# Kernel tuning notes

Measured on AMD Instinct MI355X. Metric: run time of the kernel, lower is better.

Reference implementation:

```python
import jax, jax.numpy as jnp
import numpy as np

IN_DIM = 256
OUT_DIM = 256
NUM_HEADS = 8
HEAD_DIM = OUT_DIM // NUM_HEADS
EPS = 1e-5


def setup_inputs() -> dict:
    key = jax.random.key(0)
    ks = jax.random.split(key, 12)
    B, N = 8, 1024
    s_in = 1.0 / np.sqrt(IN_DIM)
    s_out = 1.0 / np.sqrt(OUT_DIM)
    return {
        "node_features": jax.random.normal(ks[0], (B, N, IN_DIM), jnp.float32),
        "edge_weights": jax.random.uniform(ks[1], (B, N, N), jnp.float32),
        "Wq": jax.random.normal(ks[2], (IN_DIM, OUT_DIM), jnp.float32) * s_in,
        "bq": jnp.zeros((OUT_DIM,), jnp.float32),
        "Wk": jax.random.normal(ks[3], (IN_DIM, OUT_DIM), jnp.float32) * s_in,
        "bk": jnp.zeros((OUT_DIM,), jnp.float32),
        "Wv": jax.random.normal(ks[4], (IN_DIM, OUT_DIM), jnp.float32) * s_in,
        "bv": jnp.zeros((OUT_DIM,), jnp.float32),
        "We": jax.random.normal(ks[5], (NUM_HEADS,), jnp.float32),  # edge_proj: Linear(1, H)
        "be": jnp.zeros((NUM_HEADS,), jnp.float32),
        "Wo": jax.random.normal(ks[6], (OUT_DIM, OUT_DIM), jnp.float32) * s_out,
        "bo": jnp.zeros((OUT_DIM,), jnp.float32),
        "gamma": jnp.ones((OUT_DIM,), jnp.float32),
        "beta": jnp.zeros((OUT_DIM,), jnp.float32),
    }


def reference(node_features, edge_weights, Wq, bq, Wk, bk, Wv, bv, We, be, Wo, bo, gamma, beta):
    B, N, _ = node_features.shape
    H, D = NUM_HEADS, HEAD_DIM
    # QKV projections -> (B, N, H, D)
    Q = (node_features @ Wq + bq).reshape(B, N, H, D)
    K = (node_features @ Wk + bk).reshape(B, N, H, D)
    V = (node_features @ Wv + bv).reshape(B, N, H, D)
    # scores: (B, H, N, N)
    scores = jnp.einsum("bnhd,bmhd->bhnm", Q, K) / jnp.sqrt(jnp.float32(D))
    # edge bias: Linear(1->H) applied to distance matrix, permuted to (B,H,N,N)
    edge_bias = edge_weights[:, None, :, :] * We[None, :, None, None] + be[None, :, None, None]
    attn = jax.nn.softmax(scores + edge_bias, axis=-1)
    out = jnp.einsum("bhnm,bmhd->bnhd", attn, V).reshape(B, N, H * D)
    out = out @ Wo + bo
    # residual (in_dim == out_dim) + LayerNorm
    x = node_features + out
    mu = jnp.mean(x, axis=-1, keepdims=True)
    var = jnp.mean(jnp.square(x - mu), axis=-1, keepdims=True)
    return (x - mu) * jax.lax.rsqrt(var + EPS) * gamma + beta
```

## Files before the change

kernel.cpp:

```cpp
#include <hip/hip_runtime.h>

#define NB   8
#define NN   1024
#define DIN  256
#define DOUT 256
#define NH   8
#define DH   32
constexpr float LN_EPS   = 1e-5f;
constexpr float QK_SCALE = 0.17677669529663687f;

typedef __attribute__((ext_vector_type(8))) short s16x8;
typedef __attribute__((ext_vector_type(4))) float f32x4;

__device__ __forceinline__ unsigned short f2bf(float f) {
    unsigned int u = __float_as_uint(f);
    u += 0x7FFFu + ((u >> 16) & 1u);
    return (unsigned short)(u >> 16);
}
__device__ __forceinline__ float bf2f(unsigned short h) {
    return __uint_as_float(((unsigned int)h) << 16);
}
__device__ __forceinline__ unsigned int packbf(float a, float b) {
    return (unsigned int)f2bf(a) | ((unsigned int)f2bf(b) << 16);
}

__global__ __launch_bounds__(256) void qkv_kernel(
    const float* __restrict__ X,
    const float* __restrict__ Wq, const float* __restrict__ bq,
    const float* __restrict__ Wk, const float* __restrict__ bk,
    const float* __restrict__ Wv, const float* __restrict__ bv,
    unsigned short* __restrict__ Qhig, unsigned short* __restrict__ Qlog,
    unsigned short* __restrict__ Kbg,  float* __restrict__ Vf)
{
    const int m0 = blockIdx.x * 64;
    const int n0 = blockIdx.y * 64;
    const int t  = threadIdx.x;
    const int tc = t & 15, tr = t >> 4;

    __shared__ float Xs[32][68];
    __shared__ float Ws[3][32][68];

    float acc[3][4][4];
#pragma unroll
    for (int j = 0; j < 4; ++j) {
        float b0 = bq[n0 + tc*4 + j];
        float b1 = bk[n0 + tc*4 + j];
        float b2 = bv[n0 + tc*4 + j];
#pragma unroll
        for (int i = 0; i < 4; ++i) { acc[0][i][j] = b0; acc[1][i][j] = b1; acc[2][i][j] = b2; }
    }

    const int xrow = t >> 2, xseg = (t & 3) * 8;
    const int wrow = t >> 3, wseg = (t & 7) * 8;

    for (int k0 = 0; k0 < DIN; k0 += 32) {
        __syncthreads();
        {
            const float* src = X + (m0 + xrow) * DIN + k0 + xseg;
            float tmp[8];
            *(float4*)&tmp[0] = *(const float4*)(src);
            *(float4*)&tmp[4] = *(const float4*)(src + 4);
#pragma unroll
            for (int c = 0; c < 8; ++c) Xs[xseg + c][xrow] = tmp[c];
        }
#pragma unroll
        for (int w = 0; w < 3; ++w) {
            const float* Wp  = (w == 0) ? Wq : (w == 1) ? Wk : Wv;
            const float* src = Wp + (k0 + wrow) * DOUT + n0 + wseg;
            *(float4*)&Ws[w][wrow][wseg]     = *(const float4*)(src);
            *(float4*)&Ws[w][wrow][wseg + 4] = *(const float4*)(src + 4);
        }
        __syncthreads();
#pragma unroll
        for (int kk = 0; kk < 32; ++kk) {
            float4 x4 = *(const float4*)&Xs[kk][tr*4];
            float xr[4] = {x4.x, x4.y, x4.z, x4.w};
#pragma unroll
            for (int w = 0; w < 3; ++w) {
                float4 w4 = *(const float4*)&Ws[w][kk][tc*4];
                float wr[4] = {w4.x, w4.y, w4.z, w4.w};
#pragma unroll
                for (int i = 0; i < 4; ++i)
#pragma unroll
                    for (int j = 0; j < 4; ++j)
                        acc[w][i][j] = fmaf(xr[i], wr[j], acc[w][i][j]);
            }
        }
    }

    const int c0 = n0 + tc*4;
    const int h = c0 >> 5, d0 = c0 & 31;
#pragma unroll
    for (int i = 0; i < 4; ++i) {
        int row = m0 + tr*4 + i;
        int b = row >> 10, n = row & (NN - 1);
        size_t base = ((size_t)(b*NH + h)*NN + n)*DH + d0;
        ushort4 qh, ql, kb;
#pragma unroll
        for (int j = 0; j < 4; ++j) {
            float q = acc[0][i][j] * QK_SCALE;
            unsigned short hb = f2bf(q);
            float lo = q - bf2f(hb);
            ((unsigned short*)&qh)[j] = hb;
            ((unsigned short*)&ql)[j] = f2bf(lo);
            ((unsigned short*)&kb)[j] = f2bf(acc[1][i][j]);
        }
        *(ushort4*)&Qhig[base] = qh;
        *(ushort4*)&Qlog[base] = ql;
        *(ushort4*)&Kbg[base]  = kb;
        *(float4*)&Vf[base] = make_float4(acc[2][i][0], acc[2][i][1], acc[2][i][2], acc[2][i][3]);
    }
}

__global__ __launch_bounds__(256) void vtrans_kernel(
    const float* __restrict__ Vf, unsigned short* __restrict__ Vt)
{
    const int bid = blockIdx.x;
    const int c  = bid & 15;
    const int bh = bid >> 4;
    const int t  = threadIdx.x;
    __shared__ float T[64][33];
    {
        const int n = t >> 2, seg = (t & 3) * 8;
        const float* src = Vf + ((size_t)bh*NN + c*64 + n)*DH + seg;
        float4 a = *(const float4*)src;
        float4 b4 = *(const float4*)(src + 4);
        T[n][seg+0]=a.x;  T[n][seg+1]=a.y;  T[n][seg+2]=a.z;  T[n][seg+3]=a.w;
        T[n][seg+4]=b4.x; T[n][seg+5]=b4.y; T[n][seg+6]=b4.z; T[n][seg+7]=b4.w;
    }
    __syncthreads();
    {
        const int dh = t >> 3, nb = (t & 7) * 8;
        unsigned short o[8];
#pragma unroll
        for (int i = 0; i < 8; ++i) o[i] = f2bf(T[nb + i][dh]);
        *(s16x8*)&Vt[((size_t)bh*DH + dh)*NN + c*64 + nb] = *(const s16x8*)o;
    }
}

__global__ __launch_bounds__(256) void attn_kernel(
    const unsigned short* __restrict__ Qhi, const unsigned short* __restrict__ Qlo,
    const unsigned short* __restrict__ Kb,  const unsigned short* __restrict__ Vt,
    const float* __restrict__ Eg, const float* __restrict__ We,
    float* __restrict__ AO)
{
    const int bid = blockIdx.x;
    const int b  = bid & 7;
    const int h  = (bid >> 3) & 7;
    const int qt = bid >> 6;
    const int q0 = qt * 64;
    const int t    = threadIdx.x;
    const int lane = t & 63;
    const int wid  = t >> 6;
    const int l15  = lane & 15;
    const int hi   = lane >> 4;
    const int hi4  = hi * 4;

    __shared__ unsigned short Ks[64][40];
    __shared__ unsigned short Vs[32][72];
    __shared__ unsigned short Ps[4][16][72];

    const float we_h = We[h];
    const size_t kvbase = (size_t)(b*NH + h) * NN * DH;

    const int qrow = q0 + wid*16 + l15;
    const s16x8 qh_f = *(const s16x8*)(Qhi + kvbase + (size_t)qrow*DH + hi*8);
    const s16x8 ql_f = *(const s16x8*)(Qlo + kvbase + (size_t)qrow*DH + hi*8);

    const float* Ep = Eg + ((size_t)b << 20) + ((size_t)qrow << 10);

    const int krow = t >> 2, kseg = (t & 3) * 8;
    const int vrow = t >> 3, vseg = (t & 7) * 8;

    float m_run = -3.0e38f, l_run = 0.0f;
    f32x4 Oacc[2];
    Oacc[0] = (f32x4){0.f, 0.f, 0.f, 0.f};
    Oacc[1] = (f32x4){0.f, 0.f, 0.f, 0.f};

    for (int mt = 0; mt < 16; ++mt) {
        const int m0 = mt * 64;
        __syncthreads();
        *(s16x8*)&Ks[krow][kseg] = *(const s16x8*)(Kb + kvbase + (size_t)(m0 + krow)*DH + kseg);
        *(s16x8*)&Vs[vrow][vseg] = *(const s16x8*)(Vt + kvbase + (size_t)vrow*NN + m0 + vseg);
        __syncthreads();

        float s[16];
#pragma unroll
        for (int kt = 0; kt < 4; ++kt) {
            s16x8 kfr = *(const s16x8*)&Ks[kt*16 + l15][hi*8];
            f32x4 sc = (f32x4){0.f, 0.f, 0.f, 0.f};
            sc = __builtin_amdgcn_mfma_f32_16x16x32_bf16(kfr, ql_f, sc, 0, 0, 0);
            sc = __builtin_amdgcn_mfma_f32_16x16x32_bf16(kfr, qh_f, sc, 0, 0, 0);
            const float4 e4 = *(const float4*)(Ep + m0 + kt*16 + hi4);
            s[kt*4+0] = fmaf(e4.x, we_h, sc[0]);
            s[kt*4+1] = fmaf(e4.y, we_h, sc[1]);
            s[kt*4+2] = fmaf(e4.z, we_h, sc[2]);
            s[kt*4+3] = fmaf(e4.w, we_h, sc[3]);
        }

        float tm = s[0];
#pragma unroll
        for (int i = 1; i < 16; ++i) tm = fmaxf(tm, s[i]);
        tm = fmaxf(tm, __shfl_xor(tm, 16));
        tm = fmaxf(tm, __shfl_xor(tm, 32));
        const float mn = fmaxf(m_run, tm);
        const float alpha = __expf(m_run - mn);
        m_run = mn;
        float ps = 0.f;
#pragma unroll
        for (int i = 0; i < 16; ++i) { s[i] = __expf(s[i] - mn); ps += s[i]; }
        ps += __shfl_xor(ps, 16);
        ps += __shfl_xor(ps, 32);
        l_run = l_run * alpha + ps;

        const float a0 = __shfl(alpha, hi4 + 0);
        const float a1 = __shfl(alpha, hi4 + 1);
        const float a2 = __shfl(alpha, hi4 + 2);
        const float a3 = __shfl(alpha, hi4 + 3);
        Oacc[0][0] *= a0; Oacc[0][1] *= a1; Oacc[0][2] *= a2; Oacc[0][3] *= a3;
        Oacc[1][0] *= a0; Oacc[1][1] *= a1; Oacc[1][2] *= a2; Oacc[1][3] *= a3;

#pragma unroll
        for (int kt = 0; kt < 4; ++kt) {
            uint2 w;
            w.x = packbf(s[kt*4+0], s[kt*4+1]);
            w.y = packbf(s[kt*4+2], s[kt*4+3]);
            *(uint2*)&Ps[wid][l15][kt*16 + hi4] = w;
        }

#pragma unroll
        for (int c = 0; c < 2; ++c) {
            s16x8 pfr = *(const s16x8*)&Ps[wid][l15][c*32 + hi*8];
            s16x8 v0  = *(const s16x8*)&Vs[l15][c*32 + hi*8];
            s16x8 v1  = *(const s16x8*)&Vs[16 + l15][c*32 + hi*8];
            Oacc[0] = __builtin_amdgcn_mfma_f32_16x16x32_bf16(pfr, v0, Oacc[0], 0, 0, 0);
            Oacc[1] = __builtin_amdgcn_mfma_f32_16x16x32_bf16(pfr, v1, Oacc[1], 0, 0, 0);
        }
    }

    float linv[4];
#pragma unroll
    for (int r = 0; r < 4; ++r) linv[r] = 1.0f / __shfl(l_run, hi4 + r);
#pragma unroll
    for (int dt = 0; dt < 2; ++dt)
#pragma unroll
        for (int r = 0; r < 4; ++r) {
            int qg = q0 + wid*16 + hi4 + r;
            AO[((size_t)(b*NN + qg))*DOUT + h*DH + dt*16 + l15] = Oacc[dt][r] * linv[r];
        }
}

__global__ __launch_bounds__(256) void oproj_kernel(
    const float* __restrict__ A,
    const float* __restrict__ Wo, const float* __restrict__ bo,
    const float* __restrict__ X0,
    float* __restrict__ Y)
{
    const int m0 = blockIdx.x * 64;
    const int n0 = blockIdx.y * 64;
    const int t  = threadIdx.x;
    const int tc = t & 15, tr = t >> 4;

    __shared__ float As[32][68];
    __shared__ float Ws[32][68];

    float acc[4][4];
#pragma unroll
    for (int j = 0; j < 4; ++j) {
        float b0 = bo[n0 + tc*4 + j];
#pragma unroll
        for (int i = 0; i < 4; ++i) acc[i][j] = b0;
    }

    const int xrow = t >> 2, xseg = (t & 3) * 8;
    const int wrow = t >> 3, wseg = (t & 7) * 8;

    for (int k0 = 0; k0 < DOUT; k0 += 32) {
        __syncthreads();
        {
            const float* src = A + (m0 + xrow)*DOUT + k0 + xseg;
            float tmp[8];
            *(float4*)&tmp[0] = *(const float4*)(src);
            *(float4*)&tmp[4] = *(const float4*)(src + 4);
#pragma unroll
            for (int c = 0; c < 8; ++c) As[xseg + c][xrow] = tmp[c];
        }
        {
            const float* src = Wo + (k0 + wrow)*DOUT + n0 + wseg;
            *(float4*)&Ws[wrow][wseg]     = *(const float4*)(src);
            *(float4*)&Ws[wrow][wseg + 4] = *(const float4*)(src + 4);
        }
        __syncthreads();
#pragma unroll
        for (int kk = 0; kk < 32; ++kk) {
            float4 x4 = *(const float4*)&As[kk][tr*4];
            float4 w4 = *(const float4*)&Ws[kk][tc*4];
            float xr[4] = {x4.x, x4.y, x4.z, x4.w};
            float wr[4] = {w4.x, w4.y, w4.z, w4.w};
#pragma unroll
            for (int i = 0; i < 4; ++i)
#pragma unroll
                for (int j = 0; j < 4; ++j)
                    acc[i][j] = fmaf(xr[i], wr[j], acc[i][j]);
        }
    }

#pragma unroll
    for (int i = 0; i < 4; ++i) {
        int row = m0 + tr*4 + i;
        float4 r4 = *(const float4*)&X0[row*DIN + n0 + tc*4];
        float4 o;
        o.x = acc[i][0] + r4.x;
        o.y = acc[i][1] + r4.y;
        o.z = acc[i][2] + r4.z;
        o.w = acc[i][3] + r4.w;
        *(float4*)&Y[row*DOUT + n0 + tc*4] = o;
    }
}

__global__ __launch_bounds__(64) void ln_kernel(
    float* __restrict__ X, const float* __restrict__ g, const float* __restrict__ bta)
{
    const int row = blockIdx.x;
    const int l = threadIdx.x;
    float4 v = *(const float4*)&X[row*DOUT + l*4];

    float s = v.x + v.y + v.z + v.w;
#pragma unroll
    for (int m = 1; m < 64; m <<= 1) s += __shfl_xor(s, m);
    float mu = s * (1.0f / 256.0f);

    float dx = v.x - mu, dy = v.y - mu, dz = v.z - mu, dw = v.w - mu;
    float ss = dx*dx + dy*dy + dz*dz + dw*dw;
#pragma unroll
    for (int m = 1; m < 64; m <<= 1) ss += __shfl_xor(ss, m);
    float r = rsqrtf(ss * (1.0f / 256.0f) + LN_EPS);

    float4 g4 = *(const float4*)&g[l*4];
    float4 b4 = *(const float4*)&bta[l*4];
    float4 o;
    o.x = dx * r * g4.x + b4.x;
    o.y = dy * r * g4.y + b4.y;
    o.z = dz * r * g4.z + b4.z;
    o.w = dw * r * g4.w + b4.w;
    *(float4*)&X[row*DOUT + l*4] = o;
}

extern "C" void kernel_launch(void* const* d_in, const int* in_sizes, int n_in,
                              void* d_out, int out_size, void* d_ws, size_t ws_size,
                              hipStream_t stream) {
    const float* X    = (const float*)d_in[0];
    const float* E    = (const float*)d_in[1];
    const float* Wq   = (const float*)d_in[2];
    const float* bq   = (const float*)d_in[3];
    const float* Wk   = (const float*)d_in[4];
    const float* bk   = (const float*)d_in[5];
    const float* Wv   = (const float*)d_in[6];
    const float* bv   = (const float*)d_in[7];
    const float* We   = (const float*)d_in[8];
    const float* Wo   = (const float*)d_in[10];
    const float* bo   = (const float*)d_in[11];
    const float* gam  = (const float*)d_in[12];
    const float* bet  = (const float*)d_in[13];
    float* out = (float*)d_out;

    const size_t TENS = (size_t)NB * NN * DH * NH;
    unsigned short* Qhi = (unsigned short*)d_ws;
    unsigned short* Qlo = Qhi + TENS;
    unsigned short* Kb  = Qlo + TENS;
    unsigned short* Vt  = Kb + TENS;
    float* Vf = (float*)(Vt + TENS);
    float* AO = Vf + TENS;

    dim3 gA(NB*NN/64, DOUT/64);
    qkv_kernel<<<gA, 256, 0, stream>>>(X, Wq, bq, Wk, bk, Wv, bv, Qhi, Qlo, Kb, Vf);

    vtrans_kernel<<<NB*NH*(NN/64), 256, 0, stream>>>(Vf, Vt);

    attn_kernel<<<NB*NH*(NN/64), 256, 0, stream>>>(Qhi, Qlo, Kb, Vt, E, We, AO);

    dim3 gC(NB*NN/64, DOUT/64);
    oproj_kernel<<<gC, 256, 0, stream>>>(AO, Wo, bo, X, out);

    ln_kernel<<<NB*NN, 64, 0, stream>>>(out, gam, bet);
}
```

Measured before the change: 211.0 us.

## Move QKV and output projections to split-bf16 MFMA and drop LDS staging

Replaces the FP32 SIMT QKV and output-projection GEMMs with bf16 MFMA kernels that emulate FP32 precision using hi/lo splits (three MFMAs per tile). Weights and inputs are split in separate pre-kernels, the V transpose is folded into the QKV epilogue, and the attention output is written as hi/lo bf16 into reused X buffers. Attention now reads K and V fragments straight from global memory instead of staging them in LDS, and it skips the online-softmax rescale when the running max rises by at most 8. LayerNorm packs four rows per block. Costs include extra split kernels, strided scalar Vt stores, and a lazy-rescale path that relies on exp headroom.

```diff
diff --git a/kernel.cpp b/kernel.cpp
--- a/kernel.cpp
+++ b/kernel.cpp
@@ -24,174 +24,181 @@
     return (unsigned int)f2bf(a) | ((unsigned int)f2bf(b) << 16);
 }
 
-__global__ __launch_bounds__(256) void qkv_kernel(
-    const float* __restrict__ X,
-    const float* __restrict__ Wq, const float* __restrict__ bq,
-    const float* __restrict__ Wk, const float* __restrict__ bk,
-    const float* __restrict__ Wv, const float* __restrict__ bv,
-    unsigned short* __restrict__ Qhig, unsigned short* __restrict__ Qlog,
-    unsigned short* __restrict__ Kbg,  float* __restrict__ Vf)
-{
-    const int m0 = blockIdx.x * 64;
-    const int n0 = blockIdx.y * 64;
-    const int t  = threadIdx.x;
-    const int tc = t & 15, tr = t >> 4;
-
-    __shared__ float Xs[32][68];
-    __shared__ float Ws[3][32][68];
-
-    float acc[3][4][4];
-#pragma unroll
-    for (int j = 0; j < 4; ++j) {
-        float b0 = bq[n0 + tc*4 + j];
-        float b1 = bk[n0 + tc*4 + j];
-        float b2 = bv[n0 + tc*4 + j];
-#pragma unroll
-        for (int i = 0; i < 4; ++i) { acc[0][i][j] = b0; acc[1][i][j] = b1; acc[2][i][j] = b2; }
-    }
-
-    const int xrow = t >> 2, xseg = (t & 3) * 8;
-    const int wrow = t >> 3, wseg = (t & 7) * 8;
-
-    for (int k0 = 0; k0 < DIN; k0 += 32) {
-        __syncthreads();
-        {
-            const float* src = X + (m0 + xrow) * DIN + k0 + xseg;
-            float tmp[8];
-            *(float4*)&tmp[0] = *(const float4*)(src);
-            *(float4*)&tmp[4] = *(const float4*)(src + 4);
-#pragma unroll
-            for (int c = 0; c < 8; ++c) Xs[xseg + c][xrow] = tmp[c];
-        }
-#pragma unroll
-        for (int w = 0; w < 3; ++w) {
-            const float* Wp  = (w == 0) ? Wq : (w == 1) ? Wk : Wv;
-            const float* src = Wp + (k0 + wrow) * DOUT + n0 + wseg;
-            *(float4*)&Ws[w][wrow][wseg]     = *(const float4*)(src);
-            *(float4*)&Ws[w][wrow][wseg + 4] = *(const float4*)(src + 4);
-        }
-        __syncthreads();
-#pragma unroll
-        for (int kk = 0; kk < 32; ++kk) {
-            float4 x4 = *(const float4*)&Xs[kk][tr*4];
-            float xr[4] = {x4.x, x4.y, x4.z, x4.w};
-#pragma unroll
-            for (int w = 0; w < 3; ++w) {
-                float4 w4 = *(const float4*)&Ws[w][kk][tc*4];
-                float wr[4] = {w4.x, w4.y, w4.z, w4.w};
-#pragma unroll
-                for (int i = 0; i < 4; ++i)
-#pragma unroll
-                    for (int j = 0; j < 4; ++j)
-                        acc[w][i][j] = fmaf(xr[i], wr[j], acc[w][i][j]);
-            }
-        }
-    }
-
-    const int c0 = n0 + tc*4;
-    const int h = c0 >> 5, d0 = c0 & 31;
-#pragma unroll
-    for (int i = 0; i < 4; ++i) {
-        int row = m0 + tr*4 + i;
-        int b = row >> 10, n = row & (NN - 1);
-        size_t base = ((size_t)(b*NH + h)*NN + n)*DH + d0;
-        ushort4 qh, ql, kb;
-#pragma unroll
-        for (int j = 0; j < 4; ++j) {
-            float q = acc[0][i][j] * QK_SCALE;
-            unsigned short hb = f2bf(q);
-            float lo = q - bf2f(hb);
-            ((unsigned short*)&qh)[j] = hb;
-            ((unsigned short*)&ql)[j] = f2bf(lo);
-            ((unsigned short*)&kb)[j] = f2bf(acc[1][i][j]);
-        }
-        *(ushort4*)&Qhig[base] = qh;
-        *(ushort4*)&Qlog[base] = ql;
-        *(ushort4*)&Kbg[base]  = kb;
-        *(float4*)&Vf[base] = make_float4(acc[2][i][0], acc[2][i][1], acc[2][i][2], acc[2][i][3]);
-    }
-}
-
-__global__ __launch_bounds__(256) void vtrans_kernel(
-    const float* __restrict__ Vf, unsigned short* __restrict__ Vt)
-{
-    const int bid = blockIdx.x;
-    const int c  = bid & 15;
-    const int bh = bid >> 4;
-    const int t  = threadIdx.x;
-    __shared__ float T[64][33];
+__global__ __launch_bounds__(256) void wsplit_kernel(
+    const float* __restrict__ W0, const float* __restrict__ W1,
+    const float* __restrict__ W2, const float* __restrict__ W3,
+    unsigned short* __restrict__ Wt)
+{
+    const int mat = blockIdx.z;
+    const int k0 = blockIdx.x * 64, n0 = blockIdx.y * 64;
+    const float* W = (mat==0)?W0:(mat==1)?W1:(mat==2)?W2:W3;
+    __shared__ float T[64][65];
+    const int t = threadIdx.x;
     {
-        const int n = t >> 2, seg = (t & 3) * 8;
-        const float* src = Vf + ((size_t)bh*NN + c*64 + n)*DH + seg;
-        float4 a = *(const float4*)src;
-        float4 b4 = *(const float4*)(src + 4);
-        T[n][seg+0]=a.x;  T[n][seg+1]=a.y;  T[n][seg+2]=a.z;  T[n][seg+3]=a.w;
-        T[n][seg+4]=b4.x; T[n][seg+5]=b4.y; T[n][seg+6]=b4.z; T[n][seg+7]=b4.w;
+        const int r = t >> 2, cs = (t & 3) * 16;
+        const float* src = W + (k0 + r)*256 + n0 + cs;
+#pragma unroll
+        for (int i = 0; i < 4; ++i) {
+            float4 v = *(const float4*)(src + i*4);
+            T[r][cs+i*4+0] = v.x; T[r][cs+i*4+1] = v.y;
+            T[r][cs+i*4+2] = v.z; T[r][cs+i*4+3] = v.w;
+        }
     }
     __syncthreads();
     {
-        const int dh = t >> 3, nb = (t & 7) * 8;
-        unsigned short o[8];
-#pragma unroll
-        for (int i = 0; i < 8; ++i) o[i] = f2bf(T[nb + i][dh]);
-        *(s16x8*)&Vt[((size_t)bh*DH + dh)*NN + c*64 + nb] = *(const s16x8*)o;
+        const int nr = t >> 2, ks = (t & 3) * 16;
+        unsigned short hbuf[16], lbuf[16];
+#pragma unroll
+        for (int i = 0; i < 16; ++i) {
+            float x = T[ks + i][nr];
+            unsigned short hb = f2bf(x);
+            hbuf[i] = hb;
+            lbuf[i] = f2bf(x - bf2f(hb));
+        }
+        unsigned short* dh = Wt + mat*131072 + (n0+nr)*256 + k0 + ks;
+        *(s16x8*)dh           = *(const s16x8*)hbuf;
+        *(s16x8*)(dh+8)       = *(const s16x8*)(hbuf+8);
+        *(s16x8*)(dh+65536)   = *(const s16x8*)lbuf;
+        *(s16x8*)(dh+65536+8) = *(const s16x8*)(lbuf+8);
+    }
+}
+
+__global__ __launch_bounds__(256) void xsplit_kernel(
+    const float* __restrict__ X,
+    unsigned short* __restrict__ Xh, unsigned short* __restrict__ Xl)
+{
+    const size_t i = ((size_t)blockIdx.x * 256 + threadIdx.x) * 8;
+    float4 a = *(const float4*)(X + i);
+    float4 b = *(const float4*)(X + i + 4);
+    const float v[8] = {a.x, a.y, a.z, a.w, b.x, b.y, b.z, b.w};
+    unsigned short hb[8], lb[8];
+#pragma unroll
+    for (int j = 0; j < 8; ++j) {
+        hb[j] = f2bf(v[j]);
+        lb[j] = f2bf(v[j] - bf2f(hb[j]));
+    }
+    *(s16x8*)(Xh + i) = *(const s16x8*)hb;
+    *(s16x8*)(Xl + i) = *(const s16x8*)lb;
+}
+
+__global__ __launch_bounds__(256) void qkv_mfma_kernel(
+    const unsigned short* __restrict__ Xh, const unsigned short* __restrict__ Xl,
+    const unsigned short* __restrict__ Wt,
+    const float* __restrict__ bq, const float* __restrict__ bk, const float* __restrict__ bv,
+    unsigned short* __restrict__ Qh, unsigned short* __restrict__ Ql,
+    unsigned short* __restrict__ Kb, unsigned short* __restrict__ Vt)
+{
+    const int n0 = blockIdx.x * 32;
+    const int mat = blockIdx.y;
+    const int t = threadIdx.x, lane = t & 63, wid = t >> 6;
+    const int l15 = lane & 15, hi = lane >> 4, hi4 = hi * 4;
+
+    const unsigned short* Wh = Wt + mat * 131072;
+    const unsigned short* Wl = Wh + 65536;
+    const float* bias = (mat==0) ? bq : (mat==1) ? bk : bv;
+
+    f32x4 acc[4][2];
+#pragma unroll
+    for (int rt = 0; rt < 4; ++rt)
+#pragma unroll
+        for (int c = 0; c < 2; ++c) acc[rt][c] = (f32x4){0.f,0.f,0.f,0.f};
+
+#pragma unroll
+    for (int k0 = 0; k0 < 256; k0 += 32) {
+        s16x8 bhf[2], blf[2];
+#pragma unroll
+        for (int c = 0; c < 2; ++c) {
+            const size_t off = (size_t)(n0 + c*16 + l15)*256 + k0 + hi*8;
+            bhf[c] = *(const s16x8*)(Xh + off);
+            blf[c] = *(const s16x8*)(Xl + off);
+        }
+#pragma unroll
+        for (int rt = 0; rt < 4; ++rt) {
+            const size_t woff = (size_t)(wid*64 + rt*16 + l15)*256 + k0 + hi*8;
+            const s16x8 ah = *(const s16x8*)(Wh + woff);
+            const s16x8 al = *(const s16x8*)(Wl + woff);
+#pragma unroll
+            for (int c = 0; c < 2; ++c) {
+                acc[rt][c] = __builtin_amdgcn_mfma_f32_16x16x32_bf16(ah, bhf[c], acc[rt][c], 0,0,0);
+                acc[rt][c] = __builtin_amdgcn_mfma_f32_16x16x32_bf16(al, bhf[c], acc[rt][c], 0,0,0);
+                acc[rt][c] = __builtin_amdgcn_mfma_f32_16x16x32_bf16(ah, blf[c], acc[rt][c], 0,0,0);
+            }
+        }
+    }
+
+#pragma unroll
+    for (int rt = 0; rt < 4; ++rt) {
+        const int f0 = wid*64 + rt*16 + hi4;
+        const int hh = f0 >> 5, d0 = f0 & 31;
+        const float4 bs4 = *(const float4*)&bias[f0];
+        const float bsa[4] = {bs4.x, bs4.y, bs4.z, bs4.w};
+#pragma unroll
+        for (int c = 0; c < 2; ++c) {
+            const int g = n0 + c*16 + l15;
+            const int b = g >> 10, nn = g & (NN-1);
+            if (mat == 0) {
+                ushort4 qh4, ql4;
+#pragma unroll
+                for (int r = 0; r < 4; ++r) {
+                    float q = (acc[rt][c][r] + bsa[r]) * QK_SCALE;
+                    unsigned short hb = f2bf(q);
+                    ((unsigned short*)&qh4)[r] = hb;
+                    ((unsigned short*)&ql4)[r] = f2bf(q - bf2f(hb));
+                }
+                const size_t base = ((size_t)(b*NH + hh)*NN + nn)*DH + d0;
+                *(ushort4*)&Qh[base] = qh4;
+                *(ushort4*)&Ql[base] = ql4;
+            } else if (mat == 1) {
+                ushort4 kb4;
+#pragma unroll
+                for (int r = 0; r < 4; ++r)
+                    ((unsigned short*)&kb4)[r] = f2bf(acc[rt][c][r] + bsa[r]);
+                const size_t base = ((size_t)(b*NH + hh)*NN + nn)*DH + d0;
+                *(ushort4*)&Kb[base] = kb4;
+            } else {
+#pragma unroll
+                for (int r = 0; r < 4; ++r)
+                    Vt[((size_t)(b*NH + hh)*DH + d0 + r)*NN + nn] =
+                        f2bf(acc[rt][c][r] + bsa[r]);
+            }
+        }
     }
 }
 
 __global__ __launch_bounds__(256) void attn_kernel(
-    const unsigned short* __restrict__ Qhi, const unsigned short* __restrict__ Qlo,
-    const unsigned short* __restrict__ Kb,  const unsigned short* __restrict__ Vt,
+    const unsigned short* __restrict__ Qh, const unsigned short* __restrict__ Ql,
+    const unsigned short* __restrict__ Kb, const unsigned short* __restrict__ Vt,
     const float* __restrict__ Eg, const float* __restrict__ We,
-    float* __restrict__ AO)
+    unsigned short* __restrict__ AOh, unsigned short* __restrict__ AOl)
 {
     const int bid = blockIdx.x;
-    const int b  = bid & 7;
-    const int h  = (bid >> 3) & 7;
-    const int qt = bid >> 6;
+    const int b = bid & 7, h = (bid >> 3) & 7, qt = bid >> 6;
     const int q0 = qt * 64;
-    const int t    = threadIdx.x;
-    const int lane = t & 63;
-    const int wid  = t >> 6;
-    const int l15  = lane & 15;
-    const int hi   = lane >> 4;
-    const int hi4  = hi * 4;
-
-    __shared__ unsigned short Ks[64][40];
-    __shared__ unsigned short Vs[32][72];
-    __shared__ unsigned short Ps[4][16][72];
+    const int t = threadIdx.x, lane = t & 63, wid = t >> 6;
+    const int l15 = lane & 15, hi = lane >> 4, hi4 = hi * 4;
 
     const float we_h = We[h];
     const size_t kvbase = (size_t)(b*NH + h) * NN * DH;
-
     const int qrow = q0 + wid*16 + l15;
-    const s16x8 qh_f = *(const s16x8*)(Qhi + kvbase + (size_t)qrow*DH + hi*8);
-    const s16x8 ql_f = *(const s16x8*)(Qlo + kvbase + (size_t)qrow*DH + hi*8);
-
+    const s16x8 qh_f = *(const s16x8*)(Qh + kvbase + (size_t)qrow*DH + hi*8);
+    const s16x8 ql_f = *(const s16x8*)(Ql + kvbase + (size_t)qrow*DH + hi*8);
     const float* Ep = Eg + ((size_t)b << 20) + ((size_t)qrow << 10);
-
-    const int krow = t >> 2, kseg = (t & 3) * 8;
-    const int vrow = t >> 3, vseg = (t & 7) * 8;
-
-    float m_run = -3.0e38f, l_run = 0.0f;
-    f32x4 Oacc[2];
-    Oacc[0] = (f32x4){0.f, 0.f, 0.f, 0.f};
-    Oacc[1] = (f32x4){0.f, 0.f, 0.f, 0.f};
+    const int rbase = 8*(l15 >> 2) + (l15 & 3);
+
+    float m_run = -3.0e38f, l_run = 0.f;
+    f32x4 O0 = (f32x4){0.f,0.f,0.f,0.f}, O1 = (f32x4){0.f,0.f,0.f,0.f};
 
     for (int mt = 0; mt < 16; ++mt) {
         const int m0 = mt * 64;
-        __syncthreads();
-        *(s16x8*)&Ks[krow][kseg] = *(const s16x8*)(Kb + kvbase + (size_t)(m0 + krow)*DH + kseg);
-        *(s16x8*)&Vs[vrow][vseg] = *(const s16x8*)(Vt + kvbase + (size_t)vrow*NN + m0 + vseg);
-        __syncthreads();
-
         float s[16];
 #pragma unroll
         for (int kt = 0; kt < 4; ++kt) {
-            s16x8 kfr = *(const s16x8*)&Ks[kt*16 + l15][hi*8];
-            f32x4 sc = (f32x4){0.f, 0.f, 0.f, 0.f};
-            sc = __builtin_amdgcn_mfma_f32_16x16x32_bf16(kfr, ql_f, sc, 0, 0, 0);
-            sc = __builtin_amdgcn_mfma_f32_16x16x32_bf16(kfr, qh_f, sc, 0, 0, 0);
-            const float4 e4 = *(const float4*)(Ep + m0 + kt*16 + hi4);
+            const int koff = 32*(kt & 1) + 4*(kt >> 1);
+            const s16x8 kfr = *(const s16x8*)(Kb + kvbase + (size_t)(m0 + koff + rbase)*DH + hi*8);
+            f32x4 sc = (f32x4){0.f,0.f,0.f,0.f};
+            sc = __builtin_amdgcn_mfma_f32_16x16x32_bf16(kfr, ql_f, sc, 0,0,0);
+            sc = __builtin_amdgcn_mfma_f32_16x16x32_bf16(kfr, qh_f, sc, 0,0,0);
+            const float4 e4 = *(const float4*)(Ep + m0 + koff + 8*hi);
             s[kt*4+0] = fmaf(e4.x, we_h, sc[0]);
             s[kt*4+1] = fmaf(e4.y, we_h, sc[1]);
             s[kt*4+2] = fmaf(e4.z, we_h, sc[2]);
@@ -203,127 +210,131 @@
         for (int i = 1; i < 16; ++i) tm = fmaxf(tm, s[i]);
         tm = fmaxf(tm, __shfl_xor(tm, 16));
         tm = fmaxf(tm, __shfl_xor(tm, 32));
-        const float mn = fmaxf(m_run, tm);
-        const float alpha = __expf(m_run - mn);
-        m_run = mn;
+        if (!__all(tm <= m_run + 8.0f)) {
+            const float mn = fmaxf(m_run, tm);
+            const float alpha = __expf(m_run - mn);
+            m_run = mn;
+            l_run *= alpha;
+            const float a0 = __shfl(alpha, hi4+0);
+            const float a1 = __shfl(alpha, hi4+1);
+            const float a2 = __shfl(alpha, hi4+2);
+            const float a3 = __shfl(alpha, hi4+3);
+            O0[0]*=a0; O0[1]*=a1; O0[2]*=a2; O0[3]*=a3;
+            O1[0]*=a0; O1[1]*=a1; O1[2]*=a2; O1[3]*=a3;
+        }
         float ps = 0.f;
 #pragma unroll
-        for (int i = 0; i < 16; ++i) { s[i] = __expf(s[i] - mn); ps += s[i]; }
+        for (int i = 0; i < 16; ++i) { s[i] = __expf(s[i] - m_run); ps += s[i]; }
         ps += __shfl_xor(ps, 16);
         ps += __shfl_xor(ps, 32);
-        l_run = l_run * alpha + ps;
-
-        const float a0 = __shfl(alpha, hi4 + 0);
-        const float a1 = __shfl(alpha, hi4 + 1);
-        const float a2 = __shfl(alpha, hi4 + 2);
-        const float a3 = __shfl(alpha, hi4 + 3);
-        Oacc[0][0] *= a0; Oacc[0][1] *= a1; Oacc[0][2] *= a2; Oacc[0][3] *= a3;
-        Oacc[1][0] *= a0; Oacc[1][1] *= a1; Oacc[1][2] *= a2; Oacc[1][3] *= a3;
-
-#pragma unroll
-        for (int kt = 0; kt < 4; ++kt) {
-            uint2 w;
-            w.x = packbf(s[kt*4+0], s[kt*4+1]);
-            w.y = packbf(s[kt*4+2], s[kt*4+3]);
-            *(uint2*)&Ps[wid][l15][kt*16 + hi4] = w;
-        }
-
+        l_run += ps;
+
+        union { s16x8 v; unsigned int u[4]; } pf0, pf1;
+        pf0.u[0] = packbf(s[0],  s[1]);   pf0.u[1] = packbf(s[2],  s[3]);
+        pf0.u[2] = packbf(s[8],  s[9]);   pf0.u[3] = packbf(s[10], s[11]);
+        pf1.u[0] = packbf(s[4],  s[5]);   pf1.u[1] = packbf(s[6],  s[7]);
+        pf1.u[2] = packbf(s[12], s[13]);  pf1.u[3] = packbf(s[14], s[15]);
+
+        {
+            const s16x8 v00 = *(const s16x8*)(Vt + kvbase + (size_t)l15*NN      + m0      + hi*8);
+            const s16x8 v01 = *(const s16x8*)(Vt + kvbase + (size_t)(16+l15)*NN + m0      + hi*8);
+            O0 = __builtin_amdgcn_mfma_f32_16x16x32_bf16(pf0.v, v00, O0, 0,0,0);
+            O1 = __builtin_amdgcn_mfma_f32_16x16x32_bf16(pf0.v, v01, O1, 0,0,0);
+            const s16x8 v10 = *(const s16x8*)(Vt + kvbase + (size_t)l15*NN      + m0 + 32 + hi*8);
+            const s16x8 v11 = *(const s16x8*)(Vt + kvbase + (size_t)(16+l15)*NN + m0 + 32 + hi*8);
+            O0 = __builtin_amdgcn_mfma_f32_16x16x32_bf16(pf1.v, v10, O0, 0,0,0);
+            O1 = __builtin_amdgcn_mfma_f32_16x16x32_bf16(pf1.v, v11, O1, 0,0,0);
+        }
+    }
+
+    float linv[4];
+#pragma unroll
+    for (int r = 0; r < 4; ++r) linv[r] = 1.0f / __shfl(l_run, hi4 + r);
+#pragma unroll
+    for (int r = 0; r < 4; ++r) {
+        const size_t node = (size_t)b*NN + q0 + wid*16 + hi4 + r;
+        {
+            const float o = O0[r] * linv[r];
+            const unsigned short hb = f2bf(o);
+            const size_t idx = node*DOUT + h*DH + l15;
+            AOh[idx] = hb; AOl[idx] = f2bf(o - bf2f(hb));
+        }
+        {
+            const float o = O1[r] * linv[r];
+            const unsigned short hb = f2bf(o);
+            const size_t idx = node*DOUT + h*DH + 16 + l15;
+            AOh[idx] = hb; AOl[idx] = f2bf(o - bf2f(hb));
+        }
+    }
+}
+
+__global__ __launch_bounds__(256) void oproj_kernel(
+    const unsigned short* __restrict__ AOh, const unsigned short* __restrict__ AOl,
+    const unsigned short* __restrict__ Wt,
+    const float* __restrict__ bo, const float* __restrict__ X0,
+    float* __restrict__ out)
+{
+    const int n0 = blockIdx.x * 32;
+    const int fh = blockIdx.y;
+    const int t = threadIdx.x, lane = t & 63, wid = t >> 6;
+    const int l15 = lane & 15, hi = lane >> 4, hi4 = hi * 4;
+
+    const unsigned short* Wh = Wt + 3 * 131072;
+    const unsigned short* Wl = Wh + 65536;
+
+    f32x4 acc[2][2];
+#pragma unroll
+    for (int rt = 0; rt < 2; ++rt)
+#pragma unroll
+        for (int c = 0; c < 2; ++c) acc[rt][c] = (f32x4){0.f,0.f,0.f,0.f};
+
+#pragma unroll
+    for (int k0 = 0; k0 < 256; k0 += 32) {
+        s16x8 bhf[2], blf[2];
 #pragma unroll
         for (int c = 0; c < 2; ++c) {
-            s16x8 pfr = *(const s16x8*)&Ps[wid][l15][c*32 + hi*8];
-            s16x8 v0  = *(const s16x8*)&Vs[l15][c*32 + hi*8];
-            s16x8 v1  = *(const s16x8*)&Vs[16 + l15][c*32 + hi*8];
-            Oacc[0] = __builtin_amdgcn_mfma_f32_16x16x32_bf16(pfr, v0, Oacc[0], 0, 0, 0);
-            Oacc[1] = __builtin_amdgcn_mfma_f32_16x16x32_bf16(pfr, v1, Oacc[1], 0, 0, 0);
-        }
-    }
-
-    float linv[4];
-#pragma unroll
-    for (int r = 0; r < 4; ++r) linv[r] = 1.0f / __shfl(l_run, hi4 + r);
-#pragma unroll
-    for (int dt = 0; dt < 2; ++dt)
-#pragma unroll
-        for (int r = 0; r < 4; ++r) {
-            int qg = q0 + wid*16 + hi4 + r;
-            AO[((size_t)(b*NN + qg))*DOUT + h*DH + dt*16 + l15] = Oacc[dt][r] * linv[r];
-        }
-}
-
-__global__ __launch_bounds__(256) void oproj_kernel(
-    const float* __restrict__ A,
-    const float* __restrict__ Wo, const float* __restrict__ bo,
-    const float* __restrict__ X0,
-    float* __restrict__ Y)
-{
-    const int m0 = blockIdx.x * 64;
-    const int n0 = blockIdx.y * 64;
-    const int t  = threadIdx.x;
-    const int tc = t & 15, tr = t >> 4;
-
-    __shared__ float As[32][68];
-    __shared__ float Ws[32][68];
-
-    float acc[4][4];
-#pragma unroll
-    for (int j = 0; j < 4; ++j) {
-        float b0 = bo[n0 + tc*4 + j];
-#pragma unroll
-        for (int i = 0; i < 4; ++i) acc[i][j] = b0;
-    }
-
-    const int xrow = t >> 2, xseg = (t & 3) * 8;
-    const int wrow = t >> 3, wseg = (t & 7) * 8;
-
-    for (int k0 = 0; k0 < DOUT; k0 += 32) {
-        __syncthreads();
-        {
-            const float* src = A + (m0 + xrow)*DOUT + k0 + xseg;
-            float tmp[8];
-            *(float4*)&tmp[0] = *(const float4*)(src);
-            *(float4*)&tmp[4] = *(const float4*)(src + 4);
-#pragma unroll
-            for (int c = 0; c < 8; ++c) As[xseg + c][xrow] = tmp[c];
-        }
-        {
-            const float* src = Wo + (k0 + wrow)*DOUT + n0 + wseg;
-            *(float4*)&Ws[wrow][wseg]     = *(const float4*)(src);
-            *(float4*)&Ws[wrow][wseg + 4] = *(const float4*)(src + 4);
-        }
-        __syncthreads();
-#pragma unroll
-        for (int kk = 0; kk < 32; ++kk) {
-            float4 x4 = *(const float4*)&As[kk][tr*4];
-            float4 w4 = *(const float4*)&Ws[kk][tc*4];
-            float xr[4] = {x4.x, x4.y, x4.z, x4.w};
-            float wr[4] = {w4.x, w4.y, w4.z, w4.w};
-#pragma unroll
-            for (int i = 0; i < 4; ++i)
-#pragma unroll
-                for (int j = 0; j < 4; ++j)
-                    acc[i][j] = fmaf(xr[i], wr[j], acc[i][j]);
-        }
-    }
-
-#pragma unroll
-    for (int i = 0; i < 4; ++i) {
-        int row = m0 + tr*4 + i;
-        float4 r4 = *(const float4*)&X0[row*DIN + n0 + tc*4];
-        float4 o;
-        o.x = acc[i][0] + r4.x;
-        o.y = acc[i][1] + r4.y;
-        o.z = acc[i][2] + r4.z;
-        o.w = acc[i][3] + r4.w;
-        *(float4*)&Y[row*DOUT + n0 + tc*4] = o;
-    }
-}
-
-__global__ __launch_bounds__(64) void ln_kernel(
+            const size_t off = (size_t)(n0 + c*16 + l15)*256 + k0 + hi*8;
+            bhf[c] = *(const s16x8*)(AOh + off);
+            blf[c] = *(const s16x8*)(AOl + off);
+        }
+#pragma unroll
+        for (int rt = 0; rt < 2; ++rt) {
+            const size_t woff = (size_t)(fh*128 + wid*32 + rt*16 + l15)*256 + k0 + hi*8;
+            const s16x8 ah = *(const s16x8*)(Wh + woff);
+            const s16x8 al = *(const s16x8*)(Wl + woff);
+#pragma unroll
+            for (int c = 0; c < 2; ++c) {
+                acc[rt][c] = __builtin_amdgcn_mfma_f32_16x16x32_bf16(ah, bhf[c], acc[rt][c], 0,0,0);
+                acc[rt][c] = __builtin_amdgcn_mfma_f32_16x16x32_bf16(al, bhf[c], acc[rt][c], 0,0,0);
+                acc[rt][c] = __builtin_amdgcn_mfma_f32_16x16x32_bf16(ah, blf[c], acc[rt][c], 0,0,0);
+            }
+        }
+    }
+
+#pragma unroll
+    for (int rt = 0; rt < 2; ++rt) {
+        const int f0 = fh*128 + wid*32 + rt*16 + hi4;
+        const float4 bs4 = *(const float4*)&bo[f0];
+#pragma unroll
+        for (int c = 0; c < 2; ++c) {
+            const size_t g = n0 + c*16 + l15;
+            const float4 r4 = *(const float4*)&X0[g*256 + f0];
+            float4 o;
+            o.x = acc[rt][c][0] + bs4.x + r4.x;
+            o.y = acc[rt][c][1] + bs4.y + r4.y;
+            o.z = acc[rt][c][2] + bs4.z + r4.z;
+            o.w = acc[rt][c][3] + bs4.w + r4.w;
+            *(float4*)&out[g*256 + f0] = o;
+        }
+    }
+}
+
+__global__ __launch_bounds__(256) void ln_kernel(
     float* __restrict__ X, const float* __restrict__ g, const float* __restrict__ bta)
 {
-    const int row = blockIdx.x;
-    const int l = threadIdx.x;
-    float4 v = *(const float4*)&X[row*DOUT + l*4];
+    const int row = blockIdx.x * 4 + (threadIdx.x >> 6);
+    const int l = threadIdx.x & 63;
+    float4 v = *(const float4*)&X[(size_t)row*DOUT + l*4];
 
     float s = v.x + v.y + v.z + v.w;
 #pragma unroll
@@ -343,7 +354,7 @@
     o.y = dy * r * g4.y + b4.y;
     o.z = dz * r * g4.z + b4.z;
     o.w = dw * r * g4.w + b4.w;
-    *(float4*)&X[row*DOUT + l*4] = o;
+    *(float4*)&X[(size_t)row*DOUT + l*4] = o;
 }
 
 extern "C" void kernel_launch(void* const* d_in, const int* in_sizes, int n_in,
@@ -364,23 +375,20 @@
     const float* bet  = (const float*)d_in[13];
     float* out = (float*)d_out;
 
-    const size_t TENS = (size_t)NB * NN * DH * NH;
-    unsigned short* Qhi = (unsigned short*)d_ws;
-    unsigned short* Qlo = Qhi + TENS;
-    unsigned short* Kb  = Qlo + TENS;
-    unsigned short* Vt  = Kb + TENS;
-    float* Vf = (float*)(Vt + TENS);
-    float* AO = Vf + TENS;
-
-    dim3 gA(NB*NN/64, DOUT/64);
-    qkv_kernel<<<gA, 256, 0, stream>>>(X, Wq, bq, Wk, bk, Wv, bv, Qhi, Qlo, Kb, Vf);
-
-    vtrans_kernel<<<NB*NH*(NN/64), 256, 0, stream>>>(Vf, Vt);
-
-    attn_kernel<<<NB*NH*(NN/64), 256, 0, stream>>>(Qhi, Qlo, Kb, Vt, E, We, AO);
-
-    dim3 gC(NB*NN/64, DOUT/64);
-    oproj_kernel<<<gC, 256, 0, stream>>>(AO, Wo, bo, X, out);
-
-    ln_kernel<<<NB*NN, 64, 0, stream>>>(out, gam, bet);
-}
+    const size_t TENS = (size_t)NB * NN * DOUT;
+    unsigned short* SH = (unsigned short*)d_ws;
+    unsigned short* Xh = SH;
+    unsigned short* Xl = SH + TENS;
+    unsigned short* Qh = SH + 2*TENS;
+    unsigned short* Ql = SH + 3*TENS;
+    unsigned short* Kb = SH + 4*TENS;
+    unsigned short* Vt = SH + 5*TENS;
+    unsigned short* Wt = SH + 6*TENS;
+
+    wsplit_kernel<<<dim3(4,4,4), 256, 0, stream>>>(Wq, Wk, Wv, Wo, Wt);
+    xsplit_kernel<<<1024, 256, 0, stream>>>(X, Xh, Xl);
+    qkv_mfma_kernel<<<dim3(256,3), 256, 0, stream>>>(Xh, Xl, Wt, bq, bk, bv, Qh, Ql, Kb, Vt);
+    attn_kernel<<<NB*NH*(NN/64), 256, 0, stream>>>(Qh, Ql, Kb, Vt, E, We, Xh, Xl);
+    oproj_kernel<<<dim3(256,2), 256, 0, stream>>>(Xh, Xl, Wt, bo, X, out);
+    ln_kernel<<<NB*NN/4, 256, 0, stream>>>(out, gam, bet);
+}
```

Result: slower. 239.0 us (+13.2%).
